# Kernel optimization log

Hardware: AMD Instinct MI355X
Metric: run time of the kernel (lower is better)

The kernel has to match this reference:

```python
import jax, jax.numpy as jnp
import numpy as np

N_NODES = 50000


def _gcn_conv(h, W, b, src, dst, dinv):
    # PyG GCNConv: linear transform, then symmetric-normalized sum aggregation
    h = h @ W  # (N, d_out)
    norm = dinv[src] * dinv[dst]  # (E,)
    msg = h[src] * norm[:, None]  # (E, d_out)
    agg = jax.ops.segment_sum(msg, dst, num_segments=N_NODES)
    return agg + b


def setup_inputs() -> dict:
    key = jax.random.key(0)
    ks = jax.random.split(key, 9)
    in_dim, h1, h2, out_dim = 512, 512, 512, 256
    x = jax.random.normal(ks[0], (N_NODES, in_dim), dtype=jnp.float32)
    edge_index = jax.random.randint(ks[1], (2, 800000), 0, N_NODES, dtype=jnp.int64)

    def glorot(k, shape):
        lim = float(np.sqrt(6.0 / (shape[0] + shape[1])))
        return jax.random.uniform(k, shape, jnp.float32, -lim, lim)

    return {
        "x": x,
        "edge_index": edge_index,
        "W1": glorot(ks[2], (in_dim, h1)),
        "b1": jnp.zeros((h1,), jnp.float32),
        "W2": glorot(ks[3], (h1, h2)),
        "b2": jnp.zeros((h2,), jnp.float32),
        "Wout": glorot(ks[4], (h2, out_dim)),
        "bout": jnp.zeros((out_dim,), jnp.float32),
    }


def reference(x, edge_index, W1, b1, W2, b2, Wout, bout):
    # add self-loops (GCNConv default)
    loop = jnp.arange(N_NODES, dtype=edge_index.dtype)
    src = jnp.concatenate([edge_index[0], loop])
    dst = jnp.concatenate([edge_index[1], loop])
    # degree on A + I (target side), deg^{-1/2}
    deg = jax.ops.segment_sum(jnp.ones_like(dst, dtype=x.dtype), dst, num_segments=N_NODES)
    dinv = jnp.where(deg > 0, jax.lax.rsqrt(deg), 0.0)

    h = jax.nn.relu(_gcn_conv(x, W1, b1, src, dst, dinv))
    h = jax.nn.relu(_gcn_conv(h, W2, b2, src, dst, dinv))
    return h @ Wout + bout
```

## Files before the change

kernel.cpp:

```cpp
#include <hip/hip_runtime.h>

#define NN 50000
#define MP 50048
#define DD 512
#define EE 800000
#define NSCAN 196
#define SCB 3321
#define CVB 25024
#define CSRTOT (EE + NN + 3 * NN + 64)
#define CSRZB 1954

typedef unsigned short u16;
typedef __attribute__((ext_vector_type(4))) float f32x4;
typedef __attribute__((ext_vector_type(8))) __bf16 bf16x8;
typedef __attribute__((ext_vector_type(4))) short s16x4;

typedef __attribute__((address_space(1))) const void GVoid;
typedef __attribute__((address_space(3))) void LVoid;

__device__ __forceinline__ u16 f2bf(float f) {
  union { float f; unsigned u; } x; x.f = f;
  unsigned r = x.u + 0x7fffu + ((x.u >> 16) & 1u);
  return (u16)(r >> 16);
}
__device__ __forceinline__ float bf2f(u16 b) {
  union { unsigned u; float f; } x; x.u = ((unsigned)b) << 16;
  return x.f;
}


__global__ __launch_bounds__(256) void setup_k(int* __restrict__ cnt,
                                               const float* __restrict__ W1, u16* __restrict__ W1T,
                                               const float* __restrict__ W2, u16* __restrict__ W2T,
                                               const float* __restrict__ Wo, u16* __restrict__ WoT,
                                               int4* __restrict__ csr4) {
  const int b = (int)blockIdx.x, t = threadIdx.x;
  if (b < 196) { int i = b * 256 + t; if (i < NN) cnt[i] = 1; return; }
  if (b < 2756) {
    const float* W; u16* WT; int ncols, idx;
    if (b < 1220)      { W = W1; WT = W1T; ncols = 512; idx = (b - 196) * 256 + t; }
    else if (b < 2244) { W = W2; WT = W2T; ncols = 512; idx = (b - 1220) * 256 + t; }
    else               { W = Wo; WT = WoT; ncols = 256; idx = (b - 2244) * 256 + t; }
    if (idx >= 512 * ncols) return;
    int n = idx >> 9, k = idx & 511;
    WT[idx] = f2bf(W[(size_t)k * ncols + n]);
    return;
  }
  int idx = (b - 2756) * 256 + t;
  if (idx < CSRTOT / 2) csr4[idx] = make_int4(0, 0, 0, 0);
}

__global__ __launch_bounds__(256) void count_k(const int* __restrict__ dst, int* __restrict__ cnt) {
  int e = blockIdx.x * 256 + threadIdx.x;
  if (e < EE) atomicAdd(&cnt[dst[e]], 1);
}


__global__ __launch_bounds__(256) void scan1_k(const int* __restrict__ cnt, int* __restrict__ bsum) {
  __shared__ int s[256];
  const int t = threadIdx.x;
  const int i = blockIdx.x * 256 + t;
  s[t] = (i < NN) ? ((cnt[i] + 3) & ~3) : 0;
  __syncthreads();
  for (int off = 128; off > 0; off >>= 1) {
    if (t < off) s[t] += s[t + off];
    __syncthreads();
  }
  if (t == 0) bsum[blockIdx.x] = s[0];
}

__global__ __launch_bounds__(256) void scan2_k(const int* __restrict__ bsum, int* __restrict__ boff) {
  __shared__ int s[256];
  const int t = threadIdx.x;
  const int v = (t < NSCAN) ? bsum[t] : 0;
  s[t] = v;
  __syncthreads();
  for (int off = 1; off < 256; off <<= 1) {
    int a = s[t];
    int b = (t >= off) ? s[t - off] : 0;
    __syncthreads();
    s[t] = a + b;
    __syncthreads();
  }
  if (t < NSCAN) boff[t] = s[t] - v;
}

__global__ __launch_bounds__(256) void scan3_k(const int* __restrict__ cnt, const int* __restrict__ boff,
                                               int* __restrict__ rowp, int* __restrict__ cursor,
                                               float* __restrict__ dinv) {
  __shared__ int s[256];
  const int t = threadIdx.x;
  const int i = blockIdx.x * 256 + t;
  const int v = (i < NN) ? cnt[i] : 0;
  const int pv = (v + 3) & ~3;
  s[t] = pv;
  __syncthreads();
  for (int off = 1; off < 256; off <<= 1) {
    int a = s[t];
    int b = (t >= off) ? s[t - off] : 0;
    __syncthreads();
    s[t] = a + b;
    __syncthreads();
  }
  const int excl = s[t] - pv + boff[blockIdx.x];
  if (i < NN) {
    rowp[i] = excl; cursor[i] = excl;
    dinv[i] = rsqrtf((float)v);
  }
  if (i == NN - 1) rowp[NN] = excl + pv;
}


__global__ __launch_bounds__(256) void cvtscat_k(const float* __restrict__ x, u16* __restrict__ xb,
                                                 const int* __restrict__ src, const int* __restrict__ dst,
                                                 const float* __restrict__ dinv, int* __restrict__ cursor,
                                                 int2* __restrict__ csr) {
  if (blockIdx.x < SCB) {
    int e = (int)blockIdx.x * 256 + threadIdx.x;
    if (e < EE) {
      int d = dst[e], sn = src[e];
      int pos = atomicAdd(&cursor[d], 1);
      csr[pos] = make_int2(sn << 10, __float_as_int(dinv[sn] * dinv[d]));
    } else if (e < EE + NN) {
      int i = e - EE;
      int pos = atomicAdd(&cursor[i], 1);
      float di = dinv[i];
      csr[pos] = make_int2(i << 10, __float_as_int(di * di));
    }
    return;
  }
  size_t i = ((size_t)(blockIdx.x - SCB) * 256 + threadIdx.x) * 4;
  if (i >= (size_t)MP * DD) return;
  s16x4 v;
  if (i < (size_t)NN * DD) {
    f32x4 f = *(const f32x4*)(x + i);
    v = (s16x4){ (short)f2bf(f.x), (short)f2bf(f.y), (short)f2bf(f.z), (short)f2bf(f.w) };
  } else {
    v = (s16x4){ 0, 0, 0, 0 };
  }
  *(s16x4*)(xb + i) = v;
}


template<int OUT_BF16>
__global__ __launch_bounds__(256) void gemm_k(const u16* __restrict__ A, const u16* __restrict__ BT,
                                              void* __restrict__ Cv, const float* __restrict__ bias,
                                              int M, int N) {
  const int nwg = (int)gridDim.x;
  const int id = (int)blockIdx.x;
  const int xcd = id & 7;
  const int idx = id >> 3;
  const int q = nwg >> 3, r = nwg & 7;
  const int tile = (xcd < r ? xcd * (q + 1) : r * (q + 1) + (xcd - r) * q) + idx;
  const int ntn = N >> 7;
  const int bm = tile / ntn;
  const int bn = tile % ntn;

  __shared__ u16 As[2][128 * 32];
  __shared__ u16 Bs[2][128 * 32];
  const int t = threadIdx.x;
  const int lane = t & 63;
  const int wc = (t >> 6) & 1;
  const int wr = (t >> 7) & 1;
  f32x4 acc[4][4] = {};
  const int r0 = t >> 2;
  const int kc = (t & 3) * 8;
  const u16* Ab = A + (size_t)bm * 128 * DD + (size_t)r0 * DD + kc;
  const u16* Bb = BT + (size_t)bn * 128 * DD + (size_t)r0 * DD + kc;

  auto stage = [&](int buf, int kt) {
    __builtin_amdgcn_global_load_lds((GVoid*)(Ab + kt),           (LVoid*)(&As[buf][t * 8]),        16, 0, 0);
    __builtin_amdgcn_global_load_lds((GVoid*)(Ab + 64 * DD + kt), (LVoid*)(&As[buf][2048 + t * 8]), 16, 0, 0);
    __builtin_amdgcn_global_load_lds((GVoid*)(Bb + kt),           (LVoid*)(&Bs[buf][t * 8]),        16, 0, 0);
    __builtin_amdgcn_global_load_lds((GVoid*)(Bb + 64 * DD + kt), (LVoid*)(&Bs[buf][2048 + t * 8]), 16, 0, 0);
  };

  stage(0, 0);
  __syncthreads();

  #pragma unroll 2
  for (int step = 0; step < 16; ++step) {
    const int cur = step & 1;
    if (step < 15) stage(cur ^ 1, (step + 1) * 32);
    bf16x8 af[4], bv[4];
    #pragma unroll
    for (int m = 0; m < 4; ++m)
      af[m] = *(const bf16x8*)&As[cur][(wr * 64 + m * 16 + (lane & 15)) * 32 + (lane >> 4) * 8];
    #pragma unroll
    for (int n = 0; n < 4; ++n)
      bv[n] = *(const bf16x8*)&Bs[cur][(wc * 64 + n * 16 + (lane & 15)) * 32 + (lane >> 4) * 8];
    #pragma unroll
    for (int m = 0; m < 4; ++m) {
      #pragma unroll
      for (int n = 0; n < 4; ++n)
        acc[m][n] = __builtin_amdgcn_mfma_f32_16x16x32_bf16(af[m], bv[n], acc[m][n], 0, 0, 0);
    }
    __syncthreads();
  }

  const int rb = bm * 128 + wr * 64 + ((lane >> 4) * 4);
  const int cb = bn * 128 + wc * 64 + (lane & 15);
  #pragma unroll
  for (int m = 0; m < 4; ++m) {
    #pragma unroll
    for (int rr = 0; rr < 4; ++rr) {
      const int row = rb + m * 16 + rr;
      if (row < M) {
        #pragma unroll
        for (int n = 0; n < 4; ++n) {
          const int col = cb + n * 16;
          float v = acc[m][n][rr];
          if (bias) v += bias[col];
          if (OUT_BF16) ((u16*)Cv)[(size_t)row * N + col] = f2bf(v);
          else          ((float*)Cv)[(size_t)row * N + col] = v;
        }
      }
    }
  }
}


__global__ __launch_bounds__(256) void aggregate_k(const u16* __restrict__ H, const int* __restrict__ rowp,
                                                   const int2* __restrict__ csr,
                                                   const float* __restrict__ bias,
                                                   u16* __restrict__ out) {
  const int slice = (int)blockIdx.x & 7;
  const int grp = (int)blockIdx.x >> 3;
  const int wid = threadIdx.x >> 6;
  const int lane = threadIdx.x & 63;
  const int g = lane >> 4;
  const int l = lane & 15;
  const int node = grp * 16 + wid * 4 + g;
  const int d0 = slice * 64 + l * 4;
  const int beg = rowp[node];
  const int rounds = (rowp[node + 1] - beg) >> 2;
  const char* Hb = (const char*)H + (size_t)d0 * 2;
  const int4* cp = (const int4*)(csr + beg);
  float a0 = 0.f, a1 = 0.f, a2 = 0.f, a3 = 0.f;

  int4 c01 = cp[0], c23 = cp[1];
  for (int b = 0; b < rounds; ++b) {
    const s16x4 v0 = *(const s16x4*)(Hb + c01.x);
    const s16x4 v1 = *(const s16x4*)(Hb + c01.z);
    const s16x4 v2 = *(const s16x4*)(Hb + c23.x);
    const s16x4 v3 = *(const s16x4*)(Hb + c23.z);
    const int4 n01 = cp[2 * b + 2], n23 = cp[2 * b + 3];
    const float w0 = __int_as_float(c01.y), w1 = __int_as_float(c01.w);
    const float w2 = __int_as_float(c23.y), w3 = __int_as_float(c23.w);
    a0 += bf2f((u16)v0[0]) * w0 + bf2f((u16)v1[0]) * w1 + bf2f((u16)v2[0]) * w2 + bf2f((u16)v3[0]) * w3;
    a1 += bf2f((u16)v0[1]) * w0 + bf2f((u16)v1[1]) * w1 + bf2f((u16)v2[1]) * w2 + bf2f((u16)v3[1]) * w3;
    a2 += bf2f((u16)v0[2]) * w0 + bf2f((u16)v1[2]) * w1 + bf2f((u16)v2[2]) * w2 + bf2f((u16)v3[2]) * w3;
    a3 += bf2f((u16)v0[3]) * w0 + bf2f((u16)v1[3]) * w1 + bf2f((u16)v2[3]) * w2 + bf2f((u16)v3[3]) * w3;
    c01 = n01; c23 = n23;
  }

  s16x4 o;
  o[0] = (short)f2bf(fmaxf(a0 + bias[d0 + 0], 0.f));
  o[1] = (short)f2bf(fmaxf(a1 + bias[d0 + 1], 0.f));
  o[2] = (short)f2bf(fmaxf(a2 + bias[d0 + 2], 0.f));
  o[3] = (short)f2bf(fmaxf(a3 + bias[d0 + 3], 0.f));
  *(s16x4*)(out + (size_t)node * DD + d0) = o;
}


extern "C" void kernel_launch(void* const* d_in, const int* in_sizes, int n_in,
                              void* d_out, int out_size, void* d_ws, size_t ws_size,
                              hipStream_t stream) {
  const float* x    = (const float*)d_in[0];
  const int*   ei   = (const int*)d_in[1];
  const float* W1   = (const float*)d_in[2];
  const float* b1   = (const float*)d_in[3];
  const float* W2   = (const float*)d_in[4];
  const float* b2   = (const float*)d_in[5];
  const float* Wout = (const float*)d_in[6];
  const float* bout = (const float*)d_in[7];
  float* out = (float*)d_out;
  (void)in_sizes; (void)n_in; (void)out_size; (void)ws_size;

  char* ws = (char*)d_ws;
  size_t off = 0;
  auto alloc = [&](size_t bytes) -> char* {
    char* p = ws + off;
    off = (off + bytes + 255) & ~(size_t)255;
    return p;
  };
  u16*   xb   = (u16*)alloc((size_t)MP * DD * 2);
  u16*   H    = (u16*)alloc((size_t)NN * DD * 2);
  u16*   W1T  = (u16*)alloc(512 * 512 * 2);
  u16*   W2T  = (u16*)alloc(512 * 512 * 2);
  u16*   WoT  = (u16*)alloc(256 * 512 * 2);
  int*   cnt  = (int*)alloc(NN * 4);
  float* dinv = (float*)alloc(NN * 4);
  int*   rowp = (int*)alloc((NN + 1) * 4);
  int*   cur  = (int*)alloc(NN * 4);
  int2*  csr  = (int2*)alloc((size_t)CSRTOT * 8);
  int*   bsum = (int*)alloc(NSCAN * 4);
  int*   boff = (int*)alloc(NSCAN * 4);

  const int* srcp = ei;
  const int* dstp = ei + EE;

  setup_k<<<2756 + CSRZB, 256, 0, stream>>>(cnt, W1, W1T, W2, W2T, Wout, WoT, (int4*)csr);
  count_k<<<(EE + 255) / 256, 256, 0, stream>>>(dstp, cnt);
  scan1_k<<<NSCAN, 256, 0, stream>>>(cnt, bsum);
  scan2_k<<<1, 256, 0, stream>>>(bsum, boff);
  scan3_k<<<NSCAN, 256, 0, stream>>>(cnt, boff, rowp, cur, dinv);
  cvtscat_k<<<SCB + CVB, 256, 0, stream>>>(x, xb, srcp, dstp, dinv, cur, csr);

  const int agg_grid = (NN / 16) * 8;

  gemm_k<1><<<(MP / 128) * (512 / 128), 256, 0, stream>>>(xb, W1T, (void*)H, nullptr, NN, 512);
  aggregate_k<<<agg_grid, 256, 0, stream>>>(H, rowp, csr, b1, xb);
  gemm_k<1><<<(MP / 128) * (512 / 128), 256, 0, stream>>>(xb, W2T, (void*)H, nullptr, NN, 512);
  aggregate_k<<<agg_grid, 256, 0, stream>>>(H, rowp, csr, b2, xb);
  gemm_k<0><<<(MP / 128) * (256 / 128), 256, 0, stream>>>(xb, WoT, (void*)out, bout, NN, 256);
}
```

Baseline: 460.3 us.

## Fuse degree count with weight and feature conversion; widen aggregation to 8 features per lane

Degree counting, weight transpose-to-bf16 and x-to-bf16 conversion now run in one prep kernel, with the counters and CSR zeroing moved to memsets and the self-loop count added inside the scan kernels. The weight transpose now reads coalesced and writes strided. Edge scatter becomes its own kernel. The aggregation kernel has each lane handle 8 features with 16-byte loads and 32 nodes per block, giving fewer CSR index reads per feature but fewer threads in flight to hide gather latency.

```diff
diff --git a/kernel.cpp b/kernel.cpp
--- a/kernel.cpp
+++ b/kernel.cpp
@@ -6,13 +6,15 @@
 #define EE 800000
 #define NSCAN 196
 #define SCB 3321
+#define CNTB 3125
+#define WTB 2560
 #define CVB 25024
 #define CSRTOT (EE + NN + 3 * NN + 64)
-#define CSRZB 1954
 
 typedef unsigned short u16;
 typedef __attribute__((ext_vector_type(4))) float f32x4;
 typedef __attribute__((ext_vector_type(8))) __bf16 bf16x8;
+typedef __attribute__((ext_vector_type(8))) short s16x8;
 typedef __attribute__((ext_vector_type(4))) short s16x4;
 
 typedef __attribute__((address_space(1))) const void GVoid;
@@ -29,30 +31,35 @@
 }
 
 
-__global__ __launch_bounds__(256) void setup_k(int* __restrict__ cnt,
-                                               const float* __restrict__ W1, u16* __restrict__ W1T,
-                                               const float* __restrict__ W2, u16* __restrict__ W2T,
-                                               const float* __restrict__ Wo, u16* __restrict__ WoT,
-                                               int4* __restrict__ csr4) {
+__global__ __launch_bounds__(256) void prep_k(const int* __restrict__ dst, int* __restrict__ cnt,
+                                              const float* __restrict__ W1, u16* __restrict__ W1T,
+                                              const float* __restrict__ W2, u16* __restrict__ W2T,
+                                              const float* __restrict__ Wo, u16* __restrict__ WoT,
+                                              const float* __restrict__ x, u16* __restrict__ xb) {
   const int b = (int)blockIdx.x, t = threadIdx.x;
-  if (b < 196) { int i = b * 256 + t; if (i < NN) cnt[i] = 1; return; }
-  if (b < 2756) {
-    const float* W; u16* WT; int ncols, idx;
-    if (b < 1220)      { W = W1; WT = W1T; ncols = 512; idx = (b - 196) * 256 + t; }
-    else if (b < 2244) { W = W2; WT = W2T; ncols = 512; idx = (b - 1220) * 256 + t; }
-    else               { W = Wo; WT = WoT; ncols = 256; idx = (b - 2244) * 256 + t; }
-    if (idx >= 512 * ncols) return;
-    int n = idx >> 9, k = idx & 511;
-    WT[idx] = f2bf(W[(size_t)k * ncols + n]);
+  if (b < CNTB) {
+    int e = b * 256 + t;
+    atomicAdd(&cnt[dst[e]], 1);
     return;
   }
-  int idx = (b - 2756) * 256 + t;
-  if (idx < CSRTOT / 2) csr4[idx] = make_int4(0, 0, 0, 0);
-}
-
-__global__ __launch_bounds__(256) void count_k(const int* __restrict__ dst, int* __restrict__ cnt) {
-  int e = blockIdx.x * 256 + threadIdx.x;
-  if (e < EE) atomicAdd(&cnt[dst[e]], 1);
+  if (b < CNTB + WTB) {
+    int b0 = b - CNTB;
+    const float* W; u16* WT; int idx, k, n;
+    if (b0 < 1024)      { W = W1; WT = W1T; idx = b0 * 256 + t;          k = idx >> 9; n = idx & 511; WT[n * 512 + k] = f2bf(W[idx]); }
+    else if (b0 < 2048) { W = W2; WT = W2T; idx = (b0 - 1024) * 256 + t; k = idx >> 9; n = idx & 511; WT[n * 512 + k] = f2bf(W[idx]); }
+    else                { W = Wo; WT = WoT; idx = (b0 - 2048) * 256 + t; k = idx >> 8; n = idx & 255; WT[n * 512 + k] = f2bf(W[idx]); }
+    return;
+  }
+  size_t i = ((size_t)(b - CNTB - WTB) * 256 + t) * 4;
+  if (i >= (size_t)MP * DD) return;
+  s16x4 v;
+  if (i < (size_t)NN * DD) {
+    f32x4 f = *(const f32x4*)(x + i);
+    v = (s16x4){ (short)f2bf(f.x), (short)f2bf(f.y), (short)f2bf(f.z), (short)f2bf(f.w) };
+  } else {
+    v = (s16x4){ 0, 0, 0, 0 };
+  }
+  *(s16x4*)(xb + i) = v;
 }
 
 
@@ -60,7 +67,7 @@
   __shared__ int s[256];
   const int t = threadIdx.x;
   const int i = blockIdx.x * 256 + t;
-  s[t] = (i < NN) ? ((cnt[i] + 3) & ~3) : 0;
+  s[t] = (i < NN) ? ((cnt[i] + 1 + 3) & ~3) : 0;
   __syncthreads();
   for (int off = 128; off > 0; off >>= 1) {
     if (t < off) s[t] += s[t + off];
@@ -91,7 +98,7 @@
   __shared__ int s[256];
   const int t = threadIdx.x;
   const int i = blockIdx.x * 256 + t;
-  const int v = (i < NN) ? cnt[i] : 0;
+  const int v = (i < NN) ? (cnt[i] + 1) : 0;
   const int pv = (v + 3) & ~3;
   s[t] = pv;
   __syncthreads();
@@ -111,34 +118,20 @@
 }
 
 
-__global__ __launch_bounds__(256) void cvtscat_k(const float* __restrict__ x, u16* __restrict__ xb,
-                                                 const int* __restrict__ src, const int* __restrict__ dst,
+__global__ __launch_bounds__(256) void scatter_k(const int* __restrict__ src, const int* __restrict__ dst,
                                                  const float* __restrict__ dinv, int* __restrict__ cursor,
                                                  int2* __restrict__ csr) {
-  if (blockIdx.x < SCB) {
-    int e = (int)blockIdx.x * 256 + threadIdx.x;
-    if (e < EE) {
-      int d = dst[e], sn = src[e];
-      int pos = atomicAdd(&cursor[d], 1);
-      csr[pos] = make_int2(sn << 10, __float_as_int(dinv[sn] * dinv[d]));
-    } else if (e < EE + NN) {
-      int i = e - EE;
-      int pos = atomicAdd(&cursor[i], 1);
-      float di = dinv[i];
-      csr[pos] = make_int2(i << 10, __float_as_int(di * di));
-    }
-    return;
-  }
-  size_t i = ((size_t)(blockIdx.x - SCB) * 256 + threadIdx.x) * 4;
-  if (i >= (size_t)MP * DD) return;
-  s16x4 v;
-  if (i < (size_t)NN * DD) {
-    f32x4 f = *(const f32x4*)(x + i);
-    v = (s16x4){ (short)f2bf(f.x), (short)f2bf(f.y), (short)f2bf(f.z), (short)f2bf(f.w) };
-  } else {
-    v = (s16x4){ 0, 0, 0, 0 };
-  }
-  *(s16x4*)(xb + i) = v;
+  int e = (int)blockIdx.x * 256 + threadIdx.x;
+  if (e < EE) {
+    int d = dst[e], sn = src[e];
+    int pos = atomicAdd(&cursor[d], 1);
+    csr[pos] = make_int2(sn << 10, __float_as_int(dinv[sn] * dinv[d]));
+  } else if (e < EE + NN) {
+    int i = e - EE;
+    int pos = atomicAdd(&cursor[i], 1);
+    float di = dinv[i];
+    csr[pos] = make_int2(i << 10, __float_as_int(di * di));
+  }
 }
 
 
@@ -228,22 +221,23 @@
   const int grp = (int)blockIdx.x >> 3;
   const int wid = threadIdx.x >> 6;
   const int lane = threadIdx.x & 63;
-  const int g = lane >> 4;
-  const int l = lane & 15;
-  const int node = grp * 16 + wid * 4 + g;
-  const int d0 = slice * 64 + l * 4;
+  const int g = lane >> 3;
+  const int l = lane & 7;
+  const int node = grp * 32 + wid * 8 + g;
+  if (node >= NN) return;
+  const int d0 = slice * 64 + l * 8;
   const int beg = rowp[node];
   const int rounds = (rowp[node + 1] - beg) >> 2;
   const char* Hb = (const char*)H + (size_t)d0 * 2;
   const int4* cp = (const int4*)(csr + beg);
-  float a0 = 0.f, a1 = 0.f, a2 = 0.f, a3 = 0.f;
+  float a0 = 0.f, a1 = 0.f, a2 = 0.f, a3 = 0.f, a4 = 0.f, a5 = 0.f, a6 = 0.f, a7 = 0.f;
 
   int4 c01 = cp[0], c23 = cp[1];
   for (int b = 0; b < rounds; ++b) {
-    const s16x4 v0 = *(const s16x4*)(Hb + c01.x);
-    const s16x4 v1 = *(const s16x4*)(Hb + c01.z);
-    const s16x4 v2 = *(const s16x4*)(Hb + c23.x);
-    const s16x4 v3 = *(const s16x4*)(Hb + c23.z);
+    const s16x8 v0 = *(const s16x8*)(Hb + c01.x);
+    const s16x8 v1 = *(const s16x8*)(Hb + c01.z);
+    const s16x8 v2 = *(const s16x8*)(Hb + c23.x);
+    const s16x8 v3 = *(const s16x8*)(Hb + c23.z);
     const int4 n01 = cp[2 * b + 2], n23 = cp[2 * b + 3];
     const float w0 = __int_as_float(c01.y), w1 = __int_as_float(c01.w);
     const float w2 = __int_as_float(c23.y), w3 = __int_as_float(c23.w);
@@ -251,15 +245,23 @@
     a1 += bf2f((u16)v0[1]) * w0 + bf2f((u16)v1[1]) * w1 + bf2f((u16)v2[1]) * w2 + bf2f((u16)v3[1]) * w3;
     a2 += bf2f((u16)v0[2]) * w0 + bf2f((u16)v1[2]) * w1 + bf2f((u16)v2[2]) * w2 + bf2f((u16)v3[2]) * w3;
     a3 += bf2f((u16)v0[3]) * w0 + bf2f((u16)v1[3]) * w1 + bf2f((u16)v2[3]) * w2 + bf2f((u16)v3[3]) * w3;
+    a4 += bf2f((u16)v0[4]) * w0 + bf2f((u16)v1[4]) * w1 + bf2f((u16)v2[4]) * w2 + bf2f((u16)v3[4]) * w3;
+    a5 += bf2f((u16)v0[5]) * w0 + bf2f((u16)v1[5]) * w1 + bf2f((u16)v2[5]) * w2 + bf2f((u16)v3[5]) * w3;
+    a6 += bf2f((u16)v0[6]) * w0 + bf2f((u16)v1[6]) * w1 + bf2f((u16)v2[6]) * w2 + bf2f((u16)v3[6]) * w3;
+    a7 += bf2f((u16)v0[7]) * w0 + bf2f((u16)v1[7]) * w1 + bf2f((u16)v2[7]) * w2 + bf2f((u16)v3[7]) * w3;
     c01 = n01; c23 = n23;
   }
 
-  s16x4 o;
+  s16x8 o;
   o[0] = (short)f2bf(fmaxf(a0 + bias[d0 + 0], 0.f));
   o[1] = (short)f2bf(fmaxf(a1 + bias[d0 + 1], 0.f));
   o[2] = (short)f2bf(fmaxf(a2 + bias[d0 + 2], 0.f));
   o[3] = (short)f2bf(fmaxf(a3 + bias[d0 + 3], 0.f));
-  *(s16x4*)(out + (size_t)node * DD + d0) = o;
+  o[4] = (short)f2bf(fmaxf(a4 + bias[d0 + 4], 0.f));
+  o[5] = (short)f2bf(fmaxf(a5 + bias[d0 + 5], 0.f));
+  o[6] = (short)f2bf(fmaxf(a6 + bias[d0 + 6], 0.f));
+  o[7] = (short)f2bf(fmaxf(a7 + bias[d0 + 7], 0.f));
+  *(s16x8*)(out + (size_t)node * DD + d0) = o;
 }
 
 
@@ -300,14 +302,16 @@
   const int* srcp = ei;
   const int* dstp = ei + EE;
 
-  setup_k<<<2756 + CSRZB, 256, 0, stream>>>(cnt, W1, W1T, W2, W2T, Wout, WoT, (int4*)csr);
-  count_k<<<(EE + 255) / 256, 256, 0, stream>>>(dstp, cnt);
+  hipMemsetAsync(cnt, 0, NN * 4, stream);
+  hipMemsetAsync(csr, 0, (size_t)CSRTOT * 8, stream);
+
+  prep_k<<<CNTB + WTB + CVB, 256, 0, stream>>>(dstp, cnt, W1, W1T, W2, W2T, Wout, WoT, x, xb);
   scan1_k<<<NSCAN, 256, 0, stream>>>(cnt, bsum);
   scan2_k<<<1, 256, 0, stream>>>(bsum, boff);
   scan3_k<<<NSCAN, 256, 0, stream>>>(cnt, boff, rowp, cur, dinv);
-  cvtscat_k<<<SCB + CVB, 256, 0, stream>>>(x, xb, srcp, dstp, dinv, cur, csr);
-
-  const int agg_grid = (NN / 16) * 8;
+  scatter_k<<<SCB, 256, 0, stream>>>(srcp, dstp, dinv, cur, csr);
+
+  const int agg_grid = ((NN + 31) / 32) * 8;
 
   gemm_k<1><<<(MP / 128) * (512 / 128), 256, 0, stream>>>(xb, W1T, (void*)H, nullptr, NN, 512);
   aggregate_k<<<agg_grid, 256, 0, stream>>>(H, rowp, csr, b1, xb);
```

New measurement: 440.0 us. -4.4%, faster.
